# Optimization experiments

Hardware: AMD Instinct MI355X
Metric: run time of the kernel (lower is better)

The kernel has to match this reference:

```python
import jax, jax.numpy as jnp
import numpy as np

N = 50000
D = 128
E = 625000
EPS = 1e-15
BALL_EPS = 1e-5


def _logmap0(x, c):
    # Poincare ball log map at origin: artanh(sqrt(c)||x||) * x / (sqrt(c)||x||)
    sqrt_c = jnp.sqrt(c)
    xn = jnp.clip(jnp.linalg.norm(x, axis=-1, keepdims=True), EPS)
    arg = jnp.clip(sqrt_c * xn, -1.0 + BALL_EPS, 1.0 - BALL_EPS)
    return jnp.arctanh(arg) * x / (sqrt_c * xn)


def _expmap0(u, c):
    # Poincare ball exp map at origin: tanh(sqrt(c)||u||) * u / (sqrt(c)||u||)
    sqrt_c = jnp.sqrt(c)
    un = jnp.clip(jnp.linalg.norm(u, axis=-1, keepdims=True), EPS)
    return jnp.tanh(sqrt_c * un) * u / (sqrt_c * un)


def setup_inputs() -> dict:
    key = jax.random.key(0)
    ks = jax.random.split(key, 10)
    scale = 0.01  # keep points well inside the Poincare ball
    node_embeddings = jax.random.normal(ks[0], (N, D), jnp.float32) * scale
    hist1 = jax.random.normal(ks[1], (N, D), jnp.float32) * scale
    hist2 = jax.random.normal(ks[2], (N, D), jnp.float32) * scale
    hist3 = jax.random.normal(ks[3], (N, D), jnp.float32) * scale
    lin_w = jax.random.normal(ks[4], (D, D), jnp.float32) * (1.0 / np.sqrt(D))
    lin_b = jnp.zeros((D,), jnp.float32)
    conv_w = jax.random.normal(ks[5], (D, D, 3), jnp.float32) * (1.0 / np.sqrt(3 * D))
    conv_b = jnp.zeros((D,), jnp.float32)
    curvature = jnp.array([-1.0], jnp.float32)
    edge_src = jax.random.randint(ks[6], (E,), 0, N, jnp.int32)
    edge_dst = jax.random.randint(ks[7], (E,), 0, N, jnp.int32)
    return {
        'node_embeddings': node_embeddings,
        'hist1': hist1, 'hist2': hist2, 'hist3': hist3,
        'lin_w': lin_w, 'lin_b': lin_b,
        'conv_w': conv_w, 'conv_b': conv_b,
        'curvature': curvature,
        'edge_src': edge_src, 'edge_dst': edge_dst,
    }


def reference(node_embeddings, hist1, hist2, hist3, lin_w, lin_b,
              conv_w, conv_b, curvature, edge_src, edge_dst):
    c = jnp.abs(curvature[0])

    # --- HyperbolicDiffusionGraphConv ---
    tangent = _logmap0(node_embeddings, c)                       # [N, D]
    transformed = tangent @ lin_w.T + lin_b                      # [N, D]
    msgs = transformed[edge_src]                                 # [E, D] gather
    summed = jax.ops.segment_sum(msgs, edge_dst, num_segments=N)  # [N, D] scatter
    deg = jax.ops.segment_sum(jnp.ones((E,), jnp.float32), edge_dst, num_segments=N)
    neigh = jnp.where(deg[:, None] > 0, summed / jnp.clip(deg[:, None], 1.0), 0.0)
    current_emb = _expmap0(neigh, c)                             # [N, D]

    # --- HyperbolicDilatedCausalConv (3-step history, kernel_size=3 -> length 1) ---
    tangent_cur = _logmap0(current_emb, c)
    th = jnp.stack([_logmap0(hist1, c), _logmap0(hist2, c), _logmap0(hist3, c)], axis=2)  # [N, D, 3]
    # Conv1d(D -> D, k=3) on length-3 input reduces to a single contraction.
    conv_out = jnp.einsum('nik,oik->no', th, conv_w) + conv_b    # [N, D]
    return _expmap0(conv_out + tangent_cur, c)
```

## Files before the change

kernel.cpp:

```cpp
#include <hip/hip_runtime.h>
#include <hip/hip_bf16.h>

#define N_NODES 50000
#define DIM 128
#define N_EDGES 625000
#define EBLK 2442
#define SLOTS 96
#define CSTRIDE 16

#define SC_BLOCKS 25000
#define PK_BLOCKS 256
#define OT_BLOCKS (SC_BLOCKS + PK_BLOCKS)
#define IL_SPAN (EBLK * 11)
#define SB_BLOCKS (OT_BLOCKS + EBLK)

typedef float f32x4 __attribute__((ext_vector_type(4)));
typedef short s16x8 __attribute__((ext_vector_type(8)));

__device__ __forceinline__ unsigned short f2bf(float f) {
    unsigned u = __builtin_bit_cast(unsigned, f);
    unsigned r = (u + 0x7fffu + ((u >> 16) & 1u)) >> 16;
    return (unsigned short)r;
}
__device__ __forceinline__ unsigned cvtpk_bf16(float lo, float hi) {
    union { __hip_bfloat162 h; unsigned u; } cv;
    cv.h = __float22bfloat162_rn(make_float2(lo, hi));
    return cv.u;
}
__device__ __forceinline__ float lo_bf(unsigned u) {
    return __builtin_bit_cast(float, u << 16);
}
__device__ __forceinline__ float hi_bf(unsigned u) {
    return __builtin_bit_cast(float, u & 0xffff0000u);
}

__device__ __forceinline__ void gload_lds16(const unsigned short* g, unsigned short* l) {
    __builtin_amdgcn_global_load_lds(
        (const __attribute__((address_space(1))) void*)g,
        (__attribute__((address_space(3))) void*)l, 16, 0, 0);
}

__device__ __forceinline__ float logmap_scale(float ss, float sc) {
    float xn = fmaxf(sqrtf(ss), 1e-15f);
    float arg = fminf(sc * xn, 1.0f - 1e-5f);
    if (arg < 0.25f) {
        float z2 = arg * arg;
        return 1.0f + z2 * (0.33333333f + z2 * (0.2f + z2 * 0.14285715f));
    }
    float at = 0.5f * log1pf(2.0f * arg / (1.0f - arg));
    return at / (sc * xn);
}

__global__ __launch_bounds__(256) void k_sb(
    const float* __restrict__ node, const float* __restrict__ h1,
    const float* __restrict__ h2, const float* __restrict__ h3,
    const float* __restrict__ lin_w, const float* __restrict__ conv_w,
    const float* __restrict__ curv,
    const int* __restrict__ esrc, const int* __restrict__ edst,
    unsigned short* __restrict__ node_t, unsigned short* __restrict__ A,
    unsigned short* __restrict__ Wt, int* __restrict__ cnt,
    unsigned short* __restrict__ slots) {
    int b = blockIdx.x;
    int tid = threadIdx.x;
    int ot;
    if (b < IL_SPAN) {
        int q = b / 11;
        int r = b - q * 11;
        if (r == 5) {
            int e = q * 256 + tid;
            if (e < N_EDGES) {
                int d = edst[e];
                int pos = __hip_atomic_fetch_add(&cnt[d * CSTRIDE], 1,
                                                 __ATOMIC_RELAXED,
                                                 __HIP_MEMORY_SCOPE_AGENT);
                if (pos < SLOTS) slots[d * SLOTS + pos] = (unsigned short)esrc[e];
            }
            return;
        }
        ot = q * 10 + (r < 5 ? r : r - 1);
    } else {
        ot = 24420 + (b - IL_SPAN);
    }
    if (ot < SC_BLOCKS) {
        int row = ot * 8 + (tid >> 5);
        int g = tid & 31;
        int a = row / N_NODES;
        int n = row - a * N_NODES;
        const float* src = (a == 0) ? node : (a == 1) ? h1 : (a == 2) ? h2 : h3;
        float4 x = ((const float4*)&src[n * DIM])[g];
        float ss = x.x * x.x + x.y * x.y + x.z * x.z + x.w * x.w;
        ss += __shfl_xor(ss, 1, 64);
        ss += __shfl_xor(ss, 2, 64);
        ss += __shfl_xor(ss, 4, 64);
        ss += __shfl_xor(ss, 8, 64);
        ss += __shfl_xor(ss, 16, 64);
        float c = fabsf(curv[0]);
        float s = logmap_scale(ss, sqrtf(c));
        uint2 ov;
        ov.x = cvtpk_bf16(x.x * s, x.y * s);
        ov.y = cvtpk_bf16(x.z * s, x.w * s);
        if (a == 0) {
            *(uint2*)&node_t[n * DIM + g * 4] = ov;
        } else {
            *(uint2*)&A[n * 512 + a * 128 + g * 4] = ov;
        }
    } else {
        int idx = (ot - SC_BLOCKS) * 256 + tid;
        int o = idx >> 9;
        int k = idx & 511;
        float v;
        if (k < 128) {
            v = lin_w[o * 128 + k];
        } else {
            int kk = (k - 128) >> 7;
            int i = (k - 128) & 127;
            v = conv_w[o * 384 + i * 3 + kk];
        }
        Wt[idx] = f2bf(v);
    }
}

__global__ __launch_bounds__(256) void k_gather(
    const unsigned short* __restrict__ slots, const int* __restrict__ cnt,
    const unsigned short* __restrict__ node_t, unsigned short* __restrict__ A) {
    int n = blockIdx.x * 8 + (threadIdx.x >> 5);
    int lane = threadIdx.x & 31;
    int ctrue = cnt[n * CSTRIDE];
    int c = ctrue < SLOTS ? ctrue : SLOTS;
    const unsigned short* row = &slots[n * SLOTS];
    float p0 = 0.f, p1 = 0.f, p2 = 0.f, p3 = 0.f;
    float q0 = 0.f, q1 = 0.f, q2 = 0.f, q3 = 0.f;
    for (int base = 0; base < c; base += 32) {
        int rem = c - base;
        int m = rem < 32 ? rem : 32;
        int my = (int)row[base + (lane < m ? lane : m - 1)];
        for (int i = 0; i < m; i += 8) {
            int i1 = i + 1 < m ? i + 1 : m - 1;
            int i2 = i + 2 < m ? i + 2 : m - 1;
            int i3 = i + 3 < m ? i + 3 : m - 1;
            int i4 = i + 4 < m ? i + 4 : m - 1;
            int i5 = i + 5 < m ? i + 5 : m - 1;
            int i6 = i + 6 < m ? i + 6 : m - 1;
            int i7 = i + 7 < m ? i + 7 : m - 1;
            int s0 = __shfl(my, i, 32),  s1 = __shfl(my, i1, 32);
            int s2 = __shfl(my, i2, 32), s3 = __shfl(my, i3, 32);
            int s4 = __shfl(my, i4, 32), s5 = __shfl(my, i5, 32);
            int s6 = __shfl(my, i6, 32), s7 = __shfl(my, i7, 32);
            uint2 u0 = *(const uint2*)&node_t[s0 * DIM + lane * 4];
            uint2 u1 = *(const uint2*)&node_t[s1 * DIM + lane * 4];
            uint2 u2 = *(const uint2*)&node_t[s2 * DIM + lane * 4];
            uint2 u3 = *(const uint2*)&node_t[s3 * DIM + lane * 4];
            uint2 u4 = *(const uint2*)&node_t[s4 * DIM + lane * 4];
            uint2 u5 = *(const uint2*)&node_t[s5 * DIM + lane * 4];
            uint2 u6 = *(const uint2*)&node_t[s6 * DIM + lane * 4];
            uint2 u7 = *(const uint2*)&node_t[s7 * DIM + lane * 4];
            p0 += lo_bf(u0.x); p1 += hi_bf(u0.x); p2 += lo_bf(u0.y); p3 += hi_bf(u0.y);
            if (i + 1 < m) { q0 += lo_bf(u1.x); q1 += hi_bf(u1.x); q2 += lo_bf(u1.y); q3 += hi_bf(u1.y); }
            if (i + 2 < m) { p0 += lo_bf(u2.x); p1 += hi_bf(u2.x); p2 += lo_bf(u2.y); p3 += hi_bf(u2.y); }
            if (i + 3 < m) { q0 += lo_bf(u3.x); q1 += hi_bf(u3.x); q2 += lo_bf(u3.y); q3 += hi_bf(u3.y); }
            if (i + 4 < m) { p0 += lo_bf(u4.x); p1 += hi_bf(u4.x); p2 += lo_bf(u4.y); p3 += hi_bf(u4.y); }
            if (i + 5 < m) { q0 += lo_bf(u5.x); q1 += hi_bf(u5.x); q2 += lo_bf(u5.y); q3 += hi_bf(u5.y); }
            if (i + 6 < m) { p0 += lo_bf(u6.x); p1 += hi_bf(u6.x); p2 += lo_bf(u6.y); p3 += hi_bf(u6.y); }
            if (i + 7 < m) { q0 += lo_bf(u7.x); q1 += hi_bf(u7.x); q2 += lo_bf(u7.y); q3 += hi_bf(u7.y); }
        }
    }
    float t0 = p0 + q0, t1 = p1 + q1, t2 = p2 + q2, t3 = p3 + q3;
    float inv = (ctrue > 0) ? 1.0f / (float)ctrue : 0.0f;
    uint2 ov;
    ov.x = cvtpk_bf16(t0 * inv, t1 * inv);
    ov.y = cvtpk_bf16(t2 * inv, t3 * inv);
    *(uint2*)&A[n * 512 + lane * 4] = ov;
}

#define RB 128
#define BK 64
__global__ __launch_bounds__(256) void k_gemm(
    const unsigned short* __restrict__ A, const int* __restrict__ deg,
    const unsigned short* __restrict__ Wt,
    const float* __restrict__ lin_b, const float* __restrict__ conv_b,
    const float* __restrict__ curv, float* __restrict__ out) {
    __shared__ __align__(16) unsigned short As[2][RB * BK];
    __shared__ __align__(16) unsigned short Bs[2][128 * BK];
    int tid = threadIdx.x;
    int n0 = blockIdx.x * RB;
    int w = tid >> 6;
    int lane = tid & 63;
    int ml = lane & 15;
    int q = lane >> 4;
    int lr = lane >> 3;
    int lj = lane & 7;

    f32x4 acc[2][8];
    #pragma unroll
    for (int rt = 0; rt < 2; ++rt)
        #pragma unroll
        for (int i = 0; i < 8; ++i) acc[rt][i] = (f32x4){0.f, 0.f, 0.f, 0.f};

    #pragma unroll
    for (int t = 0; t < 4; ++t) {
        int m = t * 4 + w;
        int r = m * 8 + lr;
        int jg = lj ^ (r & 7);
        gload_lds16(A + (n0 + r) * 512 + jg * 8, &As[0][m * 512]);
    }
    #pragma unroll
    for (int t = 0; t < 4; ++t) {
        int m = t * 4 + w;
        int r = m * 8 + lr;
        int jg = lj ^ (r & 7);
        gload_lds16(Wt + r * 512 + jg * 8, &Bs[0][m * 512]);
    }

    #pragma unroll
    for (int kk = 0; kk < 8; ++kk) {
        int cur = kk & 1;
        __syncthreads();
        if (kk < 7) {
            int nb = cur ^ 1;
            #pragma unroll
            for (int t = 0; t < 4; ++t) {
                int m = t * 4 + w;
                int r = m * 8 + lr;
                int jg = lj ^ (r & 7);
                gload_lds16(A + (n0 + r) * 512 + (kk + 1) * 64 + jg * 8, &As[nb][m * 512]);
            }
            #pragma unroll
            for (int t = 0; t < 4; ++t) {
                int m = t * 4 + w;
                int r = m * 8 + lr;
                int jg = lj ^ (r & 7);
                gload_lds16(Wt + r * 512 + (kk + 1) * 64 + jg * 8, &Bs[nb][m * 512]);
            }
        }
        __builtin_amdgcn_s_setprio(1);
        #pragma unroll
        for (int ks = 0; ks < 2; ++ks) {
            int ca = ((ks * 4 + q) ^ (ml & 7)) * 8;
            s16x8 a0 = *(const s16x8*)&As[cur][(w * 32 + ml) * BK + ca];
            s16x8 a1 = *(const s16x8*)&As[cur][(w * 32 + 16 + ml) * BK + ca];
            #pragma unroll
            for (int ct = 0; ct < 8; ++ct) {
                s16x8 bb = *(const s16x8*)&Bs[cur][(ct * 16 + ml) * BK + ca];
                acc[0][ct] = __builtin_amdgcn_mfma_f32_16x16x32_bf16(a0, bb, acc[0][ct], 0, 0, 0);
                acc[1][ct] = __builtin_amdgcn_mfma_f32_16x16x32_bf16(a1, bb, acc[1][ct], 0, 0, 0);
            }
        }
        __builtin_amdgcn_s_setprio(0);
    }

    float c = fabsf(curv[0]);
    float sc = sqrtf(c);
    float cb[8], lb[8];
    #pragma unroll
    for (int ct = 0; ct < 8; ++ct) {
        cb[ct] = conv_b[ct * 16 + ml];
        lb[ct] = lin_b[ct * 16 + ml];
    }
    #pragma unroll
    for (int rt = 0; rt < 2; ++rt) {
        #pragma unroll
        for (int r = 0; r < 4; ++r) {
            int n = n0 + w * 32 + rt * 16 + q * 4 + r;
            bool valid = (n < N_NODES);
            float dgf = 0.f;
            if (valid) dgf = (deg[n * CSTRIDE] > 0) ? 1.0f : 0.0f;
            float y[8];
            float ssq = 0.f;
            #pragma unroll
            for (int ct = 0; ct < 8; ++ct) {
                float v = acc[rt][ct][r] + cb[ct] + dgf * lb[ct];
                y[ct] = v;
                ssq += v * v;
            }
            ssq += __shfl_xor(ssq, 1, 64);
            ssq += __shfl_xor(ssq, 2, 64);
            ssq += __shfl_xor(ssq, 4, 64);
            ssq += __shfl_xor(ssq, 8, 64);
            float un = fmaxf(sqrtf(ssq), 1e-15f);
            float z = sc * un;
            float os;
            if (z < 0.25f) {
                float z2 = z * z;
                os = 1.0f + z2 * (-0.33333333f + z2 * (0.13333333f - z2 * 0.053968254f));
            } else {
                os = tanhf(z) / z;
            }
            if (valid) {
                #pragma unroll
                for (int ct = 0; ct < 8; ++ct)
                    out[n * DIM + ct * 16 + ml] = y[ct] * os;
            }
        }
    }
}

extern "C" void kernel_launch(void* const* d_in, const int* in_sizes, int n_in,
                              void* d_out, int out_size, void* d_ws, size_t ws_size,
                              hipStream_t stream) {
    (void)in_sizes; (void)n_in; (void)out_size; (void)ws_size;
    const float* node   = (const float*)d_in[0];
    const float* h1     = (const float*)d_in[1];
    const float* h2     = (const float*)d_in[2];
    const float* h3     = (const float*)d_in[3];
    const float* lin_w  = (const float*)d_in[4];
    const float* lin_b  = (const float*)d_in[5];
    const float* conv_w = (const float*)d_in[6];
    const float* conv_b = (const float*)d_in[7];
    const float* curv   = (const float*)d_in[8];
    const int* esrc = (const int*)d_in[9];
    const int* edst = (const int*)d_in[10];
    float* out = (float*)d_out;

    char* ws = (char*)d_ws;
    unsigned short* A = (unsigned short*)ws;
    unsigned short* node_t = (unsigned short*)(ws + 51200000);
    unsigned short* Wt = (unsigned short*)(ws + 64000000);
    int* cnt = (int*)(ws + 64131072);
    unsigned short* slots = (unsigned short*)(ws + 67331072);

    (void)hipMemsetAsync(cnt, 0, N_NODES * CSTRIDE * sizeof(int), stream);
    hipLaunchKernelGGL(k_sb, dim3(SB_BLOCKS), dim3(256), 0, stream,
                       node, h1, h2, h3, lin_w, conv_w, curv, esrc, edst,
                       node_t, A, Wt, cnt, slots);
    hipLaunchKernelGGL(k_gather, dim3(6250), dim3(256), 0, stream,
                       slots, cnt, node_t, A);
    hipLaunchKernelGGL(k_gemm, dim3((N_NODES + RB - 1) / RB), dim3(256), 0, stream,
                       A, cnt, Wt, lin_b, conv_b, curv, out);
}
```

Before: 206.5 us.

## Use 16-lane 16-byte gathers and 8-wave GEMM blocks

The gather kernel now assigns 16 lanes per node, each loading 16 bytes (8 bf16) per neighbour row instead of 32 lanes loading 8 bytes, which halves the number of nodes' worth of blocks and widens memory transactions. The GEMM kernel moves to 512 threads per block, so each wave computes 16 rows instead of 32, with fewer accumulators per thread and more waves per tile. This aims at better memory-level parallelism in the gather and higher occupancy and latency hiding in the GEMM, at the cost of more per-thread accumulator registers in the gather and less B-fragment reuse per wave in the GEMM.

```diff
diff --git a/kernel.cpp b/kernel.cpp
--- a/kernel.cpp
+++ b/kernel.cpp
@@ -123,16 +123,18 @@
 __global__ __launch_bounds__(256) void k_gather(
     const unsigned short* __restrict__ slots, const int* __restrict__ cnt,
     const unsigned short* __restrict__ node_t, unsigned short* __restrict__ A) {
-    int n = blockIdx.x * 8 + (threadIdx.x >> 5);
-    int lane = threadIdx.x & 31;
+    int n = blockIdx.x * 16 + (threadIdx.x >> 4);
+    int lane = threadIdx.x & 15;
     int ctrue = cnt[n * CSTRIDE];
     int c = ctrue < SLOTS ? ctrue : SLOTS;
     const unsigned short* row = &slots[n * SLOTS];
     float p0 = 0.f, p1 = 0.f, p2 = 0.f, p3 = 0.f;
+    float p4 = 0.f, p5 = 0.f, p6 = 0.f, p7 = 0.f;
     float q0 = 0.f, q1 = 0.f, q2 = 0.f, q3 = 0.f;
-    for (int base = 0; base < c; base += 32) {
+    float q4 = 0.f, q5 = 0.f, q6 = 0.f, q7 = 0.f;
+    for (int base = 0; base < c; base += 16) {
         int rem = c - base;
-        int m = rem < 32 ? rem : 32;
+        int m = rem < 16 ? rem : 16;
         int my = (int)row[base + (lane < m ? lane : m - 1)];
         for (int i = 0; i < m; i += 8) {
             int i1 = i + 1 < m ? i + 1 : m - 1;
@@ -142,39 +144,62 @@
             int i5 = i + 5 < m ? i + 5 : m - 1;
             int i6 = i + 6 < m ? i + 6 : m - 1;
             int i7 = i + 7 < m ? i + 7 : m - 1;
-            int s0 = __shfl(my, i, 32),  s1 = __shfl(my, i1, 32);
-            int s2 = __shfl(my, i2, 32), s3 = __shfl(my, i3, 32);
-            int s4 = __shfl(my, i4, 32), s5 = __shfl(my, i5, 32);
-            int s6 = __shfl(my, i6, 32), s7 = __shfl(my, i7, 32);
-            uint2 u0 = *(const uint2*)&node_t[s0 * DIM + lane * 4];
-            uint2 u1 = *(const uint2*)&node_t[s1 * DIM + lane * 4];
-            uint2 u2 = *(const uint2*)&node_t[s2 * DIM + lane * 4];
-            uint2 u3 = *(const uint2*)&node_t[s3 * DIM + lane * 4];
-            uint2 u4 = *(const uint2*)&node_t[s4 * DIM + lane * 4];
-            uint2 u5 = *(const uint2*)&node_t[s5 * DIM + lane * 4];
-            uint2 u6 = *(const uint2*)&node_t[s6 * DIM + lane * 4];
-            uint2 u7 = *(const uint2*)&node_t[s7 * DIM + lane * 4];
+            int s0 = __shfl(my, i, 16),  s1 = __shfl(my, i1, 16);
+            int s2 = __shfl(my, i2, 16), s3 = __shfl(my, i3, 16);
+            int s4 = __shfl(my, i4, 16), s5 = __shfl(my, i5, 16);
+            int s6 = __shfl(my, i6, 16), s7 = __shfl(my, i7, 16);
+            uint4 u0 = *(const uint4*)&node_t[s0 * DIM + lane * 8];
+            uint4 u1 = *(const uint4*)&node_t[s1 * DIM + lane * 8];
+            uint4 u2 = *(const uint4*)&node_t[s2 * DIM + lane * 8];
+            uint4 u3 = *(const uint4*)&node_t[s3 * DIM + lane * 8];
+            uint4 u4 = *(const uint4*)&node_t[s4 * DIM + lane * 8];
+            uint4 u5 = *(const uint4*)&node_t[s5 * DIM + lane * 8];
+            uint4 u6 = *(const uint4*)&node_t[s6 * DIM + lane * 8];
+            uint4 u7 = *(const uint4*)&node_t[s7 * DIM + lane * 8];
             p0 += lo_bf(u0.x); p1 += hi_bf(u0.x); p2 += lo_bf(u0.y); p3 += hi_bf(u0.y);
-            if (i + 1 < m) { q0 += lo_bf(u1.x); q1 += hi_bf(u1.x); q2 += lo_bf(u1.y); q3 += hi_bf(u1.y); }
-            if (i + 2 < m) { p0 += lo_bf(u2.x); p1 += hi_bf(u2.x); p2 += lo_bf(u2.y); p3 += hi_bf(u2.y); }
-            if (i + 3 < m) { q0 += lo_bf(u3.x); q1 += hi_bf(u3.x); q2 += lo_bf(u3.y); q3 += hi_bf(u3.y); }
-            if (i + 4 < m) { p0 += lo_bf(u4.x); p1 += hi_bf(u4.x); p2 += lo_bf(u4.y); p3 += hi_bf(u4.y); }
-            if (i + 5 < m) { q0 += lo_bf(u5.x); q1 += hi_bf(u5.x); q2 += lo_bf(u5.y); q3 += hi_bf(u5.y); }
-            if (i + 6 < m) { p0 += lo_bf(u6.x); p1 += hi_bf(u6.x); p2 += lo_bf(u6.y); p3 += hi_bf(u6.y); }
-            if (i + 7 < m) { q0 += lo_bf(u7.x); q1 += hi_bf(u7.x); q2 += lo_bf(u7.y); q3 += hi_bf(u7.y); }
-        }
-    }
-    float t0 = p0 + q0, t1 = p1 + q1, t2 = p2 + q2, t3 = p3 + q3;
+            p4 += lo_bf(u0.z); p5 += hi_bf(u0.z); p6 += lo_bf(u0.w); p7 += hi_bf(u0.w);
+            if (i + 1 < m) {
+                q0 += lo_bf(u1.x); q1 += hi_bf(u1.x); q2 += lo_bf(u1.y); q3 += hi_bf(u1.y);
+                q4 += lo_bf(u1.z); q5 += hi_bf(u1.z); q6 += lo_bf(u1.w); q7 += hi_bf(u1.w);
+            }
+            if (i + 2 < m) {
+                p0 += lo_bf(u2.x); p1 += hi_bf(u2.x); p2 += lo_bf(u2.y); p3 += hi_bf(u2.y);
+                p4 += lo_bf(u2.z); p5 += hi_bf(u2.z); p6 += lo_bf(u2.w); p7 += hi_bf(u2.w);
+            }
+            if (i + 3 < m) {
+                q0 += lo_bf(u3.x); q1 += hi_bf(u3.x); q2 += lo_bf(u3.y); q3 += hi_bf(u3.y);
+                q4 += lo_bf(u3.z); q5 += hi_bf(u3.z); q6 += lo_bf(u3.w); q7 += hi_bf(u3.w);
+            }
+            if (i + 4 < m) {
+                p0 += lo_bf(u4.x); p1 += hi_bf(u4.x); p2 += lo_bf(u4.y); p3 += hi_bf(u4.y);
+                p4 += lo_bf(u4.z); p5 += hi_bf(u4.z); p6 += lo_bf(u4.w); p7 += hi_bf(u4.w);
+            }
+            if (i + 5 < m) {
+                q0 += lo_bf(u5.x); q1 += hi_bf(u5.x); q2 += lo_bf(u5.y); q3 += hi_bf(u5.y);
+                q4 += lo_bf(u5.z); q5 += hi_bf(u5.z); q6 += lo_bf(u5.w); q7 += hi_bf(u5.w);
+            }
+            if (i + 6 < m) {
+                p0 += lo_bf(u6.x); p1 += hi_bf(u6.x); p2 += lo_bf(u6.y); p3 += hi_bf(u6.y);
+                p4 += lo_bf(u6.z); p5 += hi_bf(u6.z); p6 += lo_bf(u6.w); p7 += hi_bf(u6.w);
+            }
+            if (i + 7 < m) {
+                q0 += lo_bf(u7.x); q1 += hi_bf(u7.x); q2 += lo_bf(u7.y); q3 += hi_bf(u7.y);
+                q4 += lo_bf(u7.z); q5 += hi_bf(u7.z); q6 += lo_bf(u7.w); q7 += hi_bf(u7.w);
+            }
+        }
+    }
     float inv = (ctrue > 0) ? 1.0f / (float)ctrue : 0.0f;
-    uint2 ov;
-    ov.x = cvtpk_bf16(t0 * inv, t1 * inv);
-    ov.y = cvtpk_bf16(t2 * inv, t3 * inv);
-    *(uint2*)&A[n * 512 + lane * 4] = ov;
+    uint4 ov;
+    ov.x = cvtpk_bf16((p0 + q0) * inv, (p1 + q1) * inv);
+    ov.y = cvtpk_bf16((p2 + q2) * inv, (p3 + q3) * inv);
+    ov.z = cvtpk_bf16((p4 + q4) * inv, (p5 + q5) * inv);
+    ov.w = cvtpk_bf16((p6 + q6) * inv, (p7 + q7) * inv);
+    *(uint4*)&A[n * 512 + lane * 8] = ov;
 }
 
 #define RB 128
 #define BK 64
-__global__ __launch_bounds__(256) void k_gemm(
+__global__ __launch_bounds__(512) void k_gemm(
     const unsigned short* __restrict__ A, const int* __restrict__ deg,
     const unsigned short* __restrict__ Wt,
     const float* __restrict__ lin_b, const float* __restrict__ conv_b,
@@ -190,22 +215,20 @@
     int lr = lane >> 3;
     int lj = lane & 7;
 
-    f32x4 acc[2][8];
-    #pragma unroll
-    for (int rt = 0; rt < 2; ++rt)
-        #pragma unroll
-        for (int i = 0; i < 8; ++i) acc[rt][i] = (f32x4){0.f, 0.f, 0.f, 0.f};
-
-    #pragma unroll
-    for (int t = 0; t < 4; ++t) {
-        int m = t * 4 + w;
+    f32x4 acc[8];
+    #pragma unroll
+    for (int i = 0; i < 8; ++i) acc[i] = (f32x4){0.f, 0.f, 0.f, 0.f};
+
+    #pragma unroll
+    for (int t = 0; t < 2; ++t) {
+        int m = t * 8 + w;
         int r = m * 8 + lr;
         int jg = lj ^ (r & 7);
         gload_lds16(A + (n0 + r) * 512 + jg * 8, &As[0][m * 512]);
     }
     #pragma unroll
-    for (int t = 0; t < 4; ++t) {
-        int m = t * 4 + w;
+    for (int t = 0; t < 2; ++t) {
+        int m = t * 8 + w;
         int r = m * 8 + lr;
         int jg = lj ^ (r & 7);
         gload_lds16(Wt + r * 512 + jg * 8, &Bs[0][m * 512]);
@@ -218,15 +241,15 @@
         if (kk < 7) {
             int nb = cur ^ 1;
             #pragma unroll
-            for (int t = 0; t < 4; ++t) {
-                int m = t * 4 + w;
+            for (int t = 0; t < 2; ++t) {
+                int m = t * 8 + w;
                 int r = m * 8 + lr;
                 int jg = lj ^ (r & 7);
                 gload_lds16(A + (n0 + r) * 512 + (kk + 1) * 64 + jg * 8, &As[nb][m * 512]);
             }
             #pragma unroll
-            for (int t = 0; t < 4; ++t) {
-                int m = t * 4 + w;
+            for (int t = 0; t < 2; ++t) {
+                int m = t * 8 + w;
                 int r = m * 8 + lr;
                 int jg = lj ^ (r & 7);
                 gload_lds16(Wt + r * 512 + (kk + 1) * 64 + jg * 8, &Bs[nb][m * 512]);
@@ -236,13 +259,11 @@
         #pragma unroll
         for (int ks = 0; ks < 2; ++ks) {
             int ca = ((ks * 4 + q) ^ (ml & 7)) * 8;
-            s16x8 a0 = *(const s16x8*)&As[cur][(w * 32 + ml) * BK + ca];
-            s16x8 a1 = *(const s16x8*)&As[cur][(w * 32 + 16 + ml) * BK + ca];
+            s16x8 a = *(const s16x8*)&As[cur][(w * 16 + ml) * BK + ca];
             #pragma unroll
             for (int ct = 0; ct < 8; ++ct) {
                 s16x8 bb = *(const s16x8*)&Bs[cur][(ct * 16 + ml) * BK + ca];
-                acc[0][ct] = __builtin_amdgcn_mfma_f32_16x16x32_bf16(a0, bb, acc[0][ct], 0, 0, 0);
-                acc[1][ct] = __builtin_amdgcn_mfma_f32_16x16x32_bf16(a1, bb, acc[1][ct], 0, 0, 0);
+                acc[ct] = __builtin_amdgcn_mfma_f32_16x16x32_bf16(a, bb, acc[ct], 0, 0, 0);
             }
         }
         __builtin_amdgcn_s_setprio(0);
@@ -257,39 +278,36 @@
         lb[ct] = lin_b[ct * 16 + ml];
     }
     #pragma unroll
-    for (int rt = 0; rt < 2; ++rt) {
+    for (int r = 0; r < 4; ++r) {
+        int n = n0 + w * 16 + q * 4 + r;
+        bool valid = (n < N_NODES);
+        float dgf = 0.f;
+        if (valid) dgf = (deg[n * CSTRIDE] > 0) ? 1.0f : 0.0f;
+        float y[8];
+        float ssq = 0.f;
         #pragma unroll
-        for (int r = 0; r < 4; ++r) {
-            int n = n0 + w * 32 + rt * 16 + q * 4 + r;
-            bool valid = (n < N_NODES);
-            float dgf = 0.f;
-            if (valid) dgf = (deg[n * CSTRIDE] > 0) ? 1.0f : 0.0f;
-            float y[8];
-            float ssq = 0.f;
+        for (int ct = 0; ct < 8; ++ct) {
+            float v = acc[ct][r] + cb[ct] + dgf * lb[ct];
+            y[ct] = v;
+            ssq += v * v;
+        }
+        ssq += __shfl_xor(ssq, 1, 64);
+        ssq += __shfl_xor(ssq, 2, 64);
+        ssq += __shfl_xor(ssq, 4, 64);
+        ssq += __shfl_xor(ssq, 8, 64);
+        float un = fmaxf(sqrtf(ssq), 1e-15f);
+        float z = sc * un;
+        float os;
+        if (z < 0.25f) {
+            float z2 = z * z;
+            os = 1.0f + z2 * (-0.33333333f + z2 * (0.13333333f - z2 * 0.053968254f));
+        } else {
+            os = tanhf(z) / z;
+        }
+        if (valid) {
             #pragma unroll
-            for (int ct = 0; ct < 8; ++ct) {
-                float v = acc[rt][ct][r] + cb[ct] + dgf * lb[ct];
-                y[ct] = v;
-                ssq += v * v;
-            }
-            ssq += __shfl_xor(ssq, 1, 64);
-            ssq += __shfl_xor(ssq, 2, 64);
-            ssq += __shfl_xor(ssq, 4, 64);
-            ssq += __shfl_xor(ssq, 8, 64);
-            float un = fmaxf(sqrtf(ssq), 1e-15f);
-            float z = sc * un;
-            float os;
-            if (z < 0.25f) {
-                float z2 = z * z;
-                os = 1.0f + z2 * (-0.33333333f + z2 * (0.13333333f - z2 * 0.053968254f));
-            } else {
-                os = tanhf(z) / z;
-            }
-            if (valid) {
-                #pragma unroll
-                for (int ct = 0; ct < 8; ++ct)
-                    out[n * DIM + ct * 16 + ml] = y[ct] * os;
-            }
+            for (int ct = 0; ct < 8; ++ct)
+                out[n * DIM + ct * 16 + ml] = y[ct] * os;
         }
     }
 }
@@ -322,8 +340,8 @@
     hipLaunchKernelGGL(k_sb, dim3(SB_BLOCKS), dim3(256), 0, stream,
                        node, h1, h2, h3, lin_w, conv_w, curv, esrc, edst,
                        node_t, A, Wt, cnt, slots);
-    hipLaunchKernelGGL(k_gather, dim3(6250), dim3(256), 0, stream,
+    hipLaunchKernelGGL(k_gather, dim3(3125), dim3(256), 0, stream,
                        slots, cnt, node_t, A);
-    hipLaunchKernelGGL(k_gemm, dim3((N_NODES + RB - 1) / RB), dim3(256), 0, stream,
+    hipLaunchKernelGGL(k_gemm, dim3((N_NODES + RB - 1) / RB), dim3(512), 0, stream,
                        A, cnt, Wt, lin_b, conv_b, curv, out);
 }
```

New measurement: 202.2 us. 2.1% less time.
